# Optimization experiments

Hardware: AMD Instinct MI355X
Metric: run time of the kernel (lower is better)

Reference implementation:

```python
import jax, jax.numpy as jnp
import numpy as np

C = 768
TEMB = 512
HID = int(C * 2.0)  # prompt_mlp hidden
K = max(1, int(C * 0.5))  # top-k channels = 384


def silu(x):
    return x * jax.nn.sigmoid(x)


def conv1x1(h, W, b):
    # h: [b,c,H,W], W: [o,c], b: [o]
    return jnp.einsum('bchw,oc->bohw', h, W) + b[None, :, None, None]


def setup_inputs() -> dict:
    key = jax.random.key(0)
    ks = jax.random.split(key, 20)
    s = 0.02
    return {
        'x': jax.random.normal(ks[0], (16, C, 64, 64), jnp.float32),
        'temb': jax.random.normal(ks[1], (16, TEMB), jnp.float32),
        'W_ts': jax.random.normal(ks[2], (2 * C, TEMB), jnp.float32) * s,
        'b_ts': jnp.zeros((2 * C,), jnp.float32),
        'W_tp': jax.random.normal(ks[3], (C, TEMB), jnp.float32) * s,
        'b_tp': jnp.zeros((C,), jnp.float32),
        'W_m1': jax.random.normal(ks[4], (HID, 2 * C), jnp.float32) * s,
        'b_m1': jnp.zeros((HID,), jnp.float32),
        'W_m2': jax.random.normal(ks[5], (C, HID), jnp.float32) * s,
        'b_m2': jnp.zeros((C,), jnp.float32),
        'Wq': jax.random.normal(ks[6], (C, C), jnp.float32) * s,
        'bq': jnp.zeros((C,), jnp.float32),
        'Wk': jax.random.normal(ks[7], (C, C), jnp.float32) * s,
        'bk': jnp.zeros((C,), jnp.float32),
        'Wv': jax.random.normal(ks[8], (C, C), jnp.float32) * s,
        'bv': jnp.zeros((C,), jnp.float32),
        'Wo': jax.random.normal(ks[9], (C, C), jnp.float32) * s,
        'bo': jnp.zeros((C,), jnp.float32),
    }


def reference(x, temb, W_ts, b_ts, W_tp, b_tp, W_m1, b_m1, W_m2, b_m2,
              Wq, bq, Wk, bk, Wv, bv, Wo, bo):
    b, c, H, W = x.shape
    # TimeScaleShift
    ss = silu(temb) @ W_ts.T + b_ts                       # [b, 2c]
    scale, shift = jnp.split(ss, 2, axis=1)
    h = x * (1 + scale[:, :, None, None]) + shift[:, :, None, None]
    # prompt
    gap = h.mean(axis=(2, 3))                             # [b, c]
    tp = silu(temb) @ W_tp.T + b_tp                       # [b, c]
    p = jnp.concatenate([gap, tp], axis=1)                # [b, 2c]
    prompt = silu(p @ W_m1.T + b_m1) @ W_m2.T + b_m2      # [b, c]
    # top-k channel selection
    _, idx = jax.lax.top_k(prompt, K)                     # [b, K]
    bi = jnp.arange(b)[:, None]
    # 1x1 convs then gather selected channels
    q = conv1x1(h, Wq, bq)[bi, idx].reshape(b, K, H * W)
    kf = conv1x1(h, Wk, bk)[bi, idx].reshape(b, K, H * W)
    v = conv1x1(h, Wv, bv)[bi, idx].reshape(b, K, H * W)
    # channel attention
    attn = jax.nn.softmax(jnp.einsum('bkn,bln->bkl', q, kf) * (K ** -0.5), axis=-1)
    out = jnp.einsum('bkl,bln->bkn', attn, v).reshape(b, K, H, W)
    # scatter back into full channel space
    out_full = jnp.zeros_like(h).at[bi, idx].set(out)
    return conv1x1(out_full, Wo, bo)
```

## Files before the change

### kernel.cpp

```cpp
#include <hip/hip_runtime.h>

#define NB 16
#define NC 768
#define NT 512
#define KS 384
#define NPX 4096
#define BK 64

typedef __bf16 bfx8 __attribute__((ext_vector_type(8)));
typedef float fx4 __attribute__((ext_vector_type(4)));
typedef unsigned short u16;
typedef unsigned short usv4 __attribute__((ext_vector_type(4)));

__device__ __forceinline__ u16 f2bf(float f) {
  unsigned u = __builtin_bit_cast(unsigned, f);
  u += 0x7FFFu + ((u >> 16) & 1u);
  return (u16)(u >> 16);
}

__device__ __forceinline__ void gload16(const u16* g, u16* l) {
  __builtin_amdgcn_global_load_lds(
      (const __attribute__((address_space(1))) unsigned int*)g,
      (__attribute__((address_space(3))) unsigned int*)l, 16, 0, 0);
}

__global__ void k_trans_mean(const float* __restrict__ x, u16* __restrict__ xT,
                             u16* __restrict__ xC, float* __restrict__ parts) {
  __shared__ float ld[64][65];
  int p0 = blockIdx.x * 64, c0 = blockIdx.y * 64, b = blockIdx.z;
  int t = threadIdx.x;
  int k = t & 15, ir = t >> 4;
  int jr = k * 4;
#pragma unroll
  for (int s = 0; s < 4; ++s) {
    int i = ir + s * 16;
    float4 v = *(const float4*)&x[(size_t)(b * NC + c0 + i) * NPX + p0 + jr];
    ld[i][jr] = v.x; ld[i][jr + 1] = v.y; ld[i][jr + 2] = v.z; ld[i][jr + 3] = v.w;
    usv4 pk = {f2bf(v.x), f2bf(v.y), f2bf(v.z), f2bf(v.w)};
    *(usv4*)&xC[(size_t)(b * NC + c0 + i) * NPX + p0 + jr] = pk;
  }
  __syncthreads();
#pragma unroll
  for (int s = 0; s < 4; ++s) {
    int j = ir + s * 16;
    usv4 pk = {f2bf(ld[k * 4][j]), f2bf(ld[k * 4 + 1][j]),
               f2bf(ld[k * 4 + 2][j]), f2bf(ld[k * 4 + 3][j])};
    *(usv4*)&xT[(size_t)(b * NPX + p0 + j) * NC + c0 + k * 4] = pk;
  }
  if (t < 64) {
    float s = 0.f;
    for (int j = 0; j < 64; ++j) s += ld[t][j];
    parts[(size_t)(b * NC + c0 + t) * 64 + blockIdx.x] = s;
  }
}

__global__ void k_mean_fin(const float* __restrict__ parts, float* __restrict__ xmean) {
  int id = blockIdx.x * 256 + threadIdx.x;
  if (id >= NB * NC) return;
  float s = 0.f;
  for (int j = 0; j < 64; ++j) s += parts[(size_t)id * 64 + j];
  xmean[id] = s * (1.f / 4096.f);
}

__global__ void k_silu(const float* __restrict__ temb, float* __restrict__ st) {
  int id = blockIdx.x * 256 + threadIdx.x;
  if (id < NB * NT) { float v = temb[id]; st[id] = v / (1.f + expf(-v)); }
}

__global__ void k_mlp8(const float* __restrict__ W, const float* __restrict__ bias,
                       const float* __restrict__ X, float* __restrict__ Y,
                       int len, int nj, int ostride, int obase, int dosilu) {
  __shared__ float Xs[8 * 1537];
  int t = threadIdx.x, lane = t & 63, w = t >> 6;
  int b0 = blockIdx.y * 8;
  int ldx = len + 1;
  for (int id = t; id < 8 * len; id += 256) {
    int bb = id / len, s = id - bb * len;
    Xs[bb * ldx + s] = X[(size_t)(b0 + bb) * len + s];
  }
  __syncthreads();
  for (int i = 0; i < 4; ++i) {
    int j = blockIdx.x * 16 + i * 4 + w;
    if (j < nj) {
      float acc[8] = {0, 0, 0, 0, 0, 0, 0, 0};
      for (int s = lane; s < len; s += 64) {
        float wv = W[(size_t)j * len + s];
#pragma unroll
        for (int bb = 0; bb < 8; ++bb) acc[bb] += wv * Xs[bb * ldx + s];
      }
#pragma unroll
      for (int bb = 0; bb < 8; ++bb) {
        float r = acc[bb];
#pragma unroll
        for (int m = 32; m; m >>= 1) r += __shfl_xor(r, m);
        if (lane == 0) {
          r += bias[j];
          if (dosilu) r = r / (1.f + expf(-r));
          Y[(size_t)(b0 + bb) * ostride + obase + j] = r;
        }
      }
    }
  }
}

__global__ void k_assemble_p(const float* __restrict__ Y1, const float* __restrict__ xmean,
                             float* __restrict__ p) {
  int id = blockIdx.x * 256 + threadIdx.x;
  if (id >= NB * NC) return;
  int b = id / NC, c = id - b * NC;
  const float* yb = Y1 + (size_t)b * 2304;
  p[(size_t)b * 1536 + c] = xmean[id] * (1.f + yb[c]) + yb[768 + c];
  p[(size_t)b * 1536 + 768 + c] = yb[1536 + c];
}

__global__ void k_topk(const float* __restrict__ prompt, int* __restrict__ idx) {
  __shared__ float pr[NC];
  int b = blockIdx.x, t = threadIdx.x;
  for (int c = t; c < NC; c += 256) pr[c] = prompt[(size_t)b * NC + c];
  __syncthreads();
  for (int c = t; c < NC; c += 256) {
    float v = pr[c];
    int r = 0;
    for (int c2 = 0; c2 < NC; ++c2) {
      float v2 = pr[c2];
      r += (v2 > v) || (v2 == v && c2 < c);
    }
    if (r < KS) idx[b * KS + r] = c;
  }
}

__global__ void k_fold(const int* __restrict__ idx, const float* __restrict__ Y1,
                       const float* __restrict__ xmean,
                       const float* __restrict__ Wq, const float* __restrict__ bq,
                       const float* __restrict__ Wk, const float* __restrict__ bk,
                       const float* __restrict__ Wv, const float* __restrict__ bv,
                       u16* __restrict__ Aq, float* __restrict__ biasq,
                       float* __restrict__ sig) {
  __shared__ float red[5 * 256];
  int k = blockIdx.x, b = blockIdx.y, t = threadIdx.x;
  int row = idx[b * KS + k];
  const float* yb = Y1 + (size_t)b * 2304;
  u16* aq = Aq + (size_t)b * 1152 * NC;
  float dq = 0.f, dk = 0.f, dv = 0.f, sq = 0.f, sk = 0.f;
  for (int c = t; c < NC; c += 256) {
    float sc = 1.f + yb[c], sh = yb[768 + c];
    float xm = xmean[b * NC + c];
    float wq = Wq[(size_t)row * NC + c];
    float wk = Wk[(size_t)row * NC + c];
    float wv = Wv[(size_t)row * NC + c];
    aq[(size_t)k * NC + c] = f2bf(wq * sc);
    aq[(size_t)(KS + k) * NC + c] = f2bf(wk * sc);
    aq[(size_t)(2 * KS + k) * NC + c] = f2bf(wv * sc);
    dq += wq * sh; dk += wk * sh; dv += wv * sh;
    sq += wq * sc * xm; sk += wk * sc * xm;
  }
  red[t] = dq; red[256 + t] = dk; red[512 + t] = dv; red[768 + t] = sq; red[1024 + t] = sk;
  __syncthreads();
  for (int s = 128; s; s >>= 1) {
    if (t < s) {
#pragma unroll
      for (int q = 0; q < 5; ++q) red[q * 256 + t] += red[q * 256 + t + s];
    }
    __syncthreads();
  }
  if (t == 0) {
    biasq[b * 1152 + k] = bq[row] + red[0];
    biasq[b * 1152 + KS + k] = bk[row] + red[256];
    biasq[b * 1152 + 2 * KS + k] = bv[row] + red[512];
    sig[b * NC + k] = 4096.f * red[768];
    sig[b * NC + KS + k] = 4096.f * red[1024];
  }
}

__global__ void k_gather_wo(const int* __restrict__ idx, const float* __restrict__ Wo,
                            u16* __restrict__ WoSel) {
  __shared__ int il[KS];
  int b = blockIdx.y, t = threadIdx.x;
  for (int k = t; k < KS; k += 256) il[k] = idx[b * KS + k];
  __syncthreads();
  int o0 = blockIdx.x * 8;
  for (int oo = 0; oo < 8; ++oo) {
    int o = o0 + oo;
    const float* wr = Wo + (size_t)o * NC;
    u16* dst = WoSel + ((size_t)b * NC + o) * KS;
    for (int k = t; k < KS; k += 256) dst[k] = f2bf(wr[il[k]]);
  }
}

__global__ void k_gmerge(const float* __restrict__ Gp, u16* __restrict__ G) {
  __shared__ u16 gl[128][130];
  int tt = blockIdx.x, b = blockIdx.y, t = threadIdx.x;
  int i = 0;
  while ((i + 1) * (i + 2) / 2 <= tt) ++i;
  int j = tt - i * (i + 1) / 2;
  const float* p0 = Gp + ((size_t)(0 * NB + b) * 21 + tt) * 16384;
  const float* p1 = Gp + ((size_t)(1 * NB + b) * 21 + tt) * 16384;
  const float* p2 = Gp + ((size_t)(2 * NB + b) * 21 + tt) * 16384;
#pragma unroll
  for (int s = 0; s < 16; ++s) {
    int id = t + 256 * s;
    int row = id >> 5, col4 = (id & 31) * 4;
    float4 a = *(const float4*)&p0[row * 128 + col4];
    float4 bb = *(const float4*)&p1[row * 128 + col4];
    float4 c = *(const float4*)&p2[row * 128 + col4];
    usv4 pk = {f2bf(a.x + bb.x + c.x), f2bf(a.y + bb.y + c.y),
               f2bf(a.z + bb.z + c.z), f2bf(a.w + bb.w + c.w)};
    gl[row][col4] = pk[0]; gl[row][col4 + 1] = pk[1];
    gl[row][col4 + 2] = pk[2]; gl[row][col4 + 3] = pk[3];
    *(usv4*)&G[((size_t)b * NC + i * 128 + row) * NC + j * 128 + col4] = pk;
  }
  if (i == j) return;
  __syncthreads();
#pragma unroll
  for (int s = 0; s < 16; ++s) {
    int id = t + 256 * s;
    int row = id >> 5, col4 = (id & 31) * 4;
    usv4 pk = {gl[col4][row], gl[col4 + 1][row], gl[col4 + 2][row], gl[col4 + 3][row]};
    *(usv4*)&G[((size_t)b * NC + j * 128 + row) * NC + i * 128 + col4] = pk;
  }
}

__global__ void k_softmax(const float* __restrict__ S, u16* __restrict__ At) {
  __shared__ float sh[2];
  int kk = blockIdx.x, b = blockIdx.y, t = threadIdx.x;
  const float* srow = S + ((size_t)b * KS + kk) * KS;
  float v[3];
#pragma unroll
  for (int i = 0; i < 3; ++i) v[i] = srow[t + 128 * i];
  float m = fmaxf(fmaxf(v[0], v[1]), v[2]);
#pragma unroll
  for (int s = 32; s; s >>= 1) m = fmaxf(m, __shfl_xor(m, s));
  if ((t & 63) == 0) sh[t >> 6] = m;
  __syncthreads();
  m = fmaxf(sh[0], sh[1]);
  float e[3];
  float sum = 0.f;
#pragma unroll
  for (int i = 0; i < 3; ++i) { e[i] = expf(v[i] - m); sum += e[i]; }
#pragma unroll
  for (int s = 32; s; s >>= 1) sum += __shfl_xor(sum, s);
  __syncthreads();
  if ((t & 63) == 0) sh[t >> 6] = sum;
  __syncthreads();
  sum = sh[0] + sh[1];
  float inv = 1.f / sum;
#pragma unroll
  for (int i = 0; i < 3; ++i) {
    int l = t + 128 * i;
    At[((size_t)b * KS + l) * KS + kk] = f2bf(e[i] * inv);
  }
}

template <int EPI>
__global__ __launch_bounds__(256, 2) void gemm_bt(
    const u16* __restrict__ A, const u16* __restrict__ Bt, size_t sA, size_t sB,
    int ldA, int ldB, int K, const float* __restrict__ bias, int bstride,
    float* __restrict__ outF, u16* __restrict__ outU, int ldC, size_t sC,
    const float* __restrict__ sigp, const float* __restrict__ bqp, float scale) {
  __shared__ u16 As[128 * BK];
  __shared__ u16 Bs[128 * BK];
  int b, m0, n0, kbeg = 0, kend = K, tt = 0, gpart = 0;
  if constexpr (EPI == 5) {
    tt = blockIdx.x;
    int ii = 0;
    while ((ii + 1) * (ii + 2) / 2 <= tt) ++ii;
    int jj = tt - ii * (ii + 1) / 2;
    m0 = ii * 128; n0 = jj * 128;
    b = blockIdx.z / 3; gpart = blockIdx.z % 3;
    kbeg = (gpart == 0) ? 0 : ((gpart == 1) ? 1408 : 2752);
    kend = (gpart == 0) ? 1408 : ((gpart == 1) ? 2752 : 4096);
  } else {
    b = blockIdx.z; m0 = blockIdx.y * 128; n0 = blockIdx.x * 128;
  }
  const u16* Ab = A + (size_t)b * sA;
  const u16* Bb = Bt + (size_t)b * sB;
  int t = threadIdx.x, lane = t & 63, w = t >> 6;
  int wm = (w >> 1) * 64, wn = (w & 1) * 64;
  int r16 = lane & 15, g = lane >> 4;

  int srow = w * 32 + (lane >> 3);
  int scol = (lane & 7) * 8;
  const u16* Ag = Ab + (size_t)(m0 + srow) * ldA + kbeg + scol;
  const u16* Bg = Bb + (size_t)(n0 + srow) * ldB + kbeg + scol;
  u16* Asl = &As[(w * 32) * BK];
  u16* Bsl = &Bs[(w * 32) * BK];

  fx4 acc[4][4] = {};

  for (int k0 = kbeg; k0 < kend; k0 += BK) {
#pragma unroll
    for (int s = 0; s < 4; ++s) gload16(Ag + (size_t)s * 8 * ldA, Asl + s * 8 * BK);
#pragma unroll
    for (int s = 0; s < 4; ++s) gload16(Bg + (size_t)s * 8 * ldB, Bsl + s * 8 * BK);
    Ag += BK; Bg += BK;
    __syncthreads();
#pragma unroll
    for (int kk = 0; kk < 2; ++kk) {
      bfx8 af[4], bfr[4];
#pragma unroll
      for (int i = 0; i < 4; ++i) {
        af[i] = *(const bfx8*)&As[(wm + i * 16 + r16) * BK + kk * 32 + g * 8];
        bfr[i] = *(const bfx8*)&Bs[(wn + i * 16 + r16) * BK + kk * 32 + g * 8];
      }
#pragma unroll
      for (int i = 0; i < 4; ++i)
#pragma unroll
        for (int j = 0; j < 4; ++j)
          acc[i][j] = __builtin_amdgcn_mfma_f32_16x16x32_bf16(af[i], bfr[j], acc[i][j], 0, 0, 0);
    }
    __syncthreads();
  }

#pragma unroll
  for (int i = 0; i < 4; ++i) {
#pragma unroll
    for (int j = 0; j < 4; ++j) {
      int row = wm + i * 16 + g * 4;
      int col = wn + j * 16 + r16;
      fx4 v = acc[i][j];
      if constexpr (EPI == 0) {
        usv4 pk;
#pragma unroll
        for (int r = 0; r < 4; ++r) pk[r] = f2bf(v[r] + bias[b * bstride + m0 + row + r]);
        *(usv4*)&outU[(size_t)b * sC + (size_t)(n0 + col) * ldC + (m0 + row)] = pk;
      } else if constexpr (EPI == 1) {
        int gc = n0 + col;
        float bk_ = bqp[b * 1152 + 384 + gc];
        float sk_ = sigp[b * NC + 384 + gc];
#pragma unroll
        for (int r = 0; r < 4; ++r) {
          int gr = m0 + row + r;
          float bq_ = bqp[b * 1152 + gr];
          float sq_ = sigp[b * NC + gr];
          float val = (v[r] + bq_ * sk_ + bk_ * sq_ + 4096.f * bq_ * bk_) * scale;
          outF[(size_t)b * sC + (size_t)gr * ldC + gc] = val;
        }
      } else if constexpr (EPI == 2) {
#pragma unroll
        for (int r = 0; r < 4; ++r)
          outU[(size_t)b * sC + (size_t)(m0 + row + r) * ldC + (n0 + col)] = f2bf(v[r]);
      } else if constexpr (EPI == 3) {
#pragma unroll
        for (int r = 0; r < 4; ++r)
          outF[(size_t)b * sC + (size_t)(m0 + row + r) * ldC + (n0 + col)] =
              v[r] + bias[b * bstride + m0 + row + r];
      } else {
        float* o = outF + ((size_t)(gpart * NB + b) * 21 + tt) * 16384;
#pragma unroll
        for (int r = 0; r < 4; ++r) o[(row + r) * 128 + col] = v[r];
      }
    }
  }
}

__global__ void k_sentinel(float* out, int n) {
  int id = blockIdx.x * 256 + threadIdx.x;
  if (id < n) out[id] = 12345.0f;
}

extern "C" void kernel_launch(void* const* d_in, const int* in_sizes, int n_in,
                              void* d_out, int out_size, void* d_ws, size_t ws_size,
                              hipStream_t stream) {
  const float* x    = (const float*)d_in[0];
  const float* temb = (const float*)d_in[1];
  const float* W_ts = (const float*)d_in[2];
  const float* b_ts = (const float*)d_in[3];
  const float* W_tp = (const float*)d_in[4];
  const float* b_tp = (const float*)d_in[5];
  const float* W_m1 = (const float*)d_in[6];
  const float* b_m1 = (const float*)d_in[7];
  const float* W_m2 = (const float*)d_in[8];
  const float* b_m2 = (const float*)d_in[9];
  const float* Wq = (const float*)d_in[10];
  const float* bq = (const float*)d_in[11];
  const float* Wk = (const float*)d_in[12];
  const float* bk = (const float*)d_in[13];
  const float* Wv = (const float*)d_in[14];
  const float* bv = (const float*)d_in[15];
  const float* Wo = (const float*)d_in[16];
  const float* bo = (const float*)d_in[17];
  float* out = (float*)d_out;

  char* base = (char*)d_ws;
  size_t off = 0;
  auto alloc = [&](size_t bytes) -> char* {
    char* pp = base + off;
    off += (bytes + 255) & ~(size_t)255;
    return pp;
  };
  u16* xT   = (u16*)alloc((size_t)NB * NPX * NC * 2);
  u16* xC   = (u16*)alloc((size_t)NB * NC * NPX * 2);
  u16* vT   = (u16*)alloc((size_t)NB * NPX * KS * 2);
  u16* Aq   = (u16*)alloc((size_t)NB * 1152 * NC * 2);
  u16* WoS  = (u16*)alloc((size_t)NB * NC * KS * 2);
  float* parts  = (float*)alloc((size_t)NB * NC * 64 * 4);
  float* xmean  = (float*)alloc((size_t)NB * NC * 4);
  float* Y1     = (float*)alloc((size_t)NB * 2304 * 4);
  float* st     = (float*)alloc((size_t)NB * NT * 4);
  float* p      = (float*)alloc((size_t)NB * 1536 * 4);
  float* hid    = (float*)alloc((size_t)NB * 1536 * 4);
  float* pr     = (float*)alloc((size_t)NB * NC * 4);
  int*   idx    = (int*)alloc((size_t)NB * KS * 4);
  float* biasq  = (float*)alloc((size_t)NB * 1152 * 4);
  float* sig    = (float*)alloc((size_t)NB * NC * 4);

  if (off > ws_size) {
    k_sentinel<<<(out_size + 255) / 256, 256, 0, stream>>>(out, out_size);
    return;
  }

  float* Gp = (float*)xT;
  u16* G  = (u16*)xC;
  u16* T  = (u16*)((char*)xC + 20u * 1024 * 1024);
  float* S = (float*)((char*)xC + 30u * 1024 * 1024);
  u16* At = (u16*)((char*)xC + 40u * 1024 * 1024);
  u16* Mm = (u16*)((char*)xC + 46u * 1024 * 1024);

  k_trans_mean<<<dim3(64, 12, NB), 256, 0, stream>>>(x, xT, xC, parts);
  k_mean_fin<<<(NB * NC + 255) / 256, 256, 0, stream>>>(parts, xmean);
  k_silu<<<(NB * NT + 255) / 256, 256, 0, stream>>>(temb, st);
  k_mlp8<<<dim3(96, 2), 256, 0, stream>>>(W_ts, b_ts, st, Y1, 512, 1536, 2304, 0, 0);
  k_mlp8<<<dim3(48, 2), 256, 0, stream>>>(W_tp, b_tp, st, Y1, 512, 768, 2304, 1536, 0);
  k_assemble_p<<<(NB * NC + 255) / 256, 256, 0, stream>>>(Y1, xmean, p);
  k_mlp8<<<dim3(96, 2), 256, 0, stream>>>(W_m1, b_m1, p, hid, 1536, 1536, 1536, 0, 1);
  k_mlp8<<<dim3(48, 2), 256, 0, stream>>>(W_m2, b_m2, hid, pr, 1536, 768, 768, 0, 0);
  k_topk<<<NB, 256, 0, stream>>>(pr, idx);
  k_fold<<<dim3(KS, NB), 256, 0, stream>>>(idx, Y1, xmean, Wq, bq, Wk, bk, Wv, bv, Aq, biasq, sig);
  k_gather_wo<<<dim3(96, NB), 256, 0, stream>>>(idx, Wo, WoS);

  gemm_bt<0><<<dim3(32, 3, NB), 256, 0, stream>>>(
      Aq + (size_t)2 * KS * NC, xT, (size_t)1152 * NC, (size_t)NPX * NC, NC, NC, NC,
      biasq + 2 * KS, 1152, nullptr, vT, KS, (size_t)NPX * KS, nullptr, nullptr, 0.f);
  gemm_bt<5><<<dim3(21, 1, NB * 3), 256, 0, stream>>>(
      xC, xC, (size_t)NC * NPX, (size_t)NC * NPX, NPX, NPX, NPX,
      nullptr, 0, Gp, nullptr, 0, 0, nullptr, nullptr, 0.f);
  k_gmerge<<<dim3(21, NB), 256, 0, stream>>>(Gp, G);
  gemm_bt<2><<<dim3(6, 3, NB), 256, 0, stream>>>(
      Aq + (size_t)KS * NC, G, (size_t)1152 * NC, (size_t)NC * NC, NC, NC, NC,
      nullptr, 0, nullptr, T, NC, (size_t)KS * NC, nullptr, nullptr, 0.f);
  gemm_bt<1><<<dim3(3, 3, NB), 256, 0, stream>>>(
      Aq, T, (size_t)1152 * NC, (size_t)KS * NC, NC, NC, NC,
      nullptr, 0, S, nullptr, KS, (size_t)KS * KS, sig, biasq, 0.05103103630798287f);
  k_softmax<<<dim3(KS, NB), 128, 0, stream>>>(S, At);
  gemm_bt<2><<<dim3(3, 6, NB), 256, 0, stream>>>(
      WoS, At, (size_t)NC * KS, (size_t)KS * KS, KS, KS, KS,
      nullptr, 0, nullptr, Mm, KS, (size_t)NC * KS, nullptr, nullptr, 0.f);
  gemm_bt<3><<<dim3(32, 6, NB), 256, 0, stream>>>(
      Mm, vT, (size_t)NC * KS, (size_t)NPX * KS, KS, KS, KS,
      bo, 0, out, nullptr, NPX, (size_t)NC * NPX, nullptr, nullptr, 0.f);
}
```

Before: 675.4 us.

## Fold V projection into output weights and drop separate V GEMM

Instead of materialising the projected V tensor over all pixels, the kernel multiplies Wo-selected weights by the attention matrix and then by the scaled V weights. This yields a per-batch 768x768 combined weight, applied directly to the transposed input in one GEMM, with a separately computed fused bias. It also reduces the Gram split-K from three parts to two and merges the mean-finalize and SiLU kernels. The change removes the V GEMM and its intermediate traffic, but the final GEMM's reduction dimension doubles to 768 and it adds a transpose and a small GEMM.

```diff
diff --git a/kernel.cpp b/kernel.cpp
--- a/kernel.cpp
+++ b/kernel.cpp
@@ -16,6 +16,9 @@
   unsigned u = __builtin_bit_cast(unsigned, f);
   u += 0x7FFFu + ((u >> 16) & 1u);
   return (u16)(u >> 16);
+}
+__device__ __forceinline__ float bf2f(u16 v) {
+  return __builtin_bit_cast(float, (unsigned)v << 16);
 }
 
 __device__ __forceinline__ void gload16(const u16* g, u16* l) {
@@ -54,17 +57,15 @@
   }
 }
 
-__global__ void k_mean_fin(const float* __restrict__ parts, float* __restrict__ xmean) {
-  int id = blockIdx.x * 256 + threadIdx.x;
-  if (id >= NB * NC) return;
-  float s = 0.f;
-  for (int j = 0; j < 64; ++j) s += parts[(size_t)id * 64 + j];
-  xmean[id] = s * (1.f / 4096.f);
-}
-
-__global__ void k_silu(const float* __restrict__ temb, float* __restrict__ st) {
+__global__ void k_misc(const float* __restrict__ parts, float* __restrict__ xmean,
+                       const float* __restrict__ temb, float* __restrict__ st) {
   int id = blockIdx.x * 256 + threadIdx.x;
   if (id < NB * NT) { float v = temb[id]; st[id] = v / (1.f + expf(-v)); }
+  if (id < NB * NC) {
+    float s = 0.f;
+    for (int j = 0; j < 64; ++j) s += parts[(size_t)id * 64 + j];
+    xmean[id] = s * (1.f / 4096.f);
+  }
 }
 
 __global__ void k_mlp8(const float* __restrict__ W, const float* __restrict__ bias,
@@ -134,13 +135,14 @@
                        const float* __restrict__ Wq, const float* __restrict__ bq,
                        const float* __restrict__ Wk, const float* __restrict__ bk,
                        const float* __restrict__ Wv, const float* __restrict__ bv,
-                       u16* __restrict__ Aq, float* __restrict__ biasq,
-                       float* __restrict__ sig) {
+                       u16* __restrict__ Aq, u16* __restrict__ Avtmp,
+                       float* __restrict__ biasq, float* __restrict__ sig) {
   __shared__ float red[5 * 256];
   int k = blockIdx.x, b = blockIdx.y, t = threadIdx.x;
   int row = idx[b * KS + k];
   const float* yb = Y1 + (size_t)b * 2304;
-  u16* aq = Aq + (size_t)b * 1152 * NC;
+  u16* aq = Aq + (size_t)b * 768 * NC;
+  u16* av = Avtmp + (size_t)b * KS * NC;
   float dq = 0.f, dk = 0.f, dv = 0.f, sq = 0.f, sk = 0.f;
   for (int c = t; c < NC; c += 256) {
     float sc = 1.f + yb[c], sh = yb[768 + c];
@@ -150,7 +152,7 @@
     float wv = Wv[(size_t)row * NC + c];
     aq[(size_t)k * NC + c] = f2bf(wq * sc);
     aq[(size_t)(KS + k) * NC + c] = f2bf(wk * sc);
-    aq[(size_t)(2 * KS + k) * NC + c] = f2bf(wv * sc);
+    av[(size_t)k * NC + c] = f2bf(wv * sc);
     dq += wq * sh; dk += wk * sh; dv += wv * sh;
     sq += wq * sc * xm; sk += wk * sc * xm;
   }
@@ -169,6 +171,25 @@
     biasq[b * 1152 + 2 * KS + k] = bv[row] + red[512];
     sig[b * NC + k] = 4096.f * red[768];
     sig[b * NC + KS + k] = 4096.f * red[1024];
+  }
+}
+
+__global__ void k_avt(const u16* __restrict__ Avtmp, u16* __restrict__ AvT) {
+  __shared__ u16 tl[64][65];
+  int lt = blockIdx.x % 6, ct = blockIdx.x / 6, b = blockIdx.y;
+  int l0 = lt * 64, c0 = ct * 64, t = threadIdx.x;
+#pragma unroll
+  for (int s = 0; s < 16; ++s) {
+    int id = t + 256 * s;
+    int r = id >> 6, c = id & 63;
+    tl[r][c] = Avtmp[(size_t)b * KS * NC + (size_t)(l0 + r) * NC + c0 + c];
+  }
+  __syncthreads();
+#pragma unroll
+  for (int s = 0; s < 16; ++s) {
+    int id = t + 256 * s;
+    int r = id >> 6, c = id & 63;
+    AvT[(size_t)b * NC * KS + (size_t)(c0 + r) * KS + l0 + c] = tl[c][r];
   }
 }
 
@@ -195,16 +216,13 @@
   int j = tt - i * (i + 1) / 2;
   const float* p0 = Gp + ((size_t)(0 * NB + b) * 21 + tt) * 16384;
   const float* p1 = Gp + ((size_t)(1 * NB + b) * 21 + tt) * 16384;
-  const float* p2 = Gp + ((size_t)(2 * NB + b) * 21 + tt) * 16384;
 #pragma unroll
   for (int s = 0; s < 16; ++s) {
     int id = t + 256 * s;
     int row = id >> 5, col4 = (id & 31) * 4;
     float4 a = *(const float4*)&p0[row * 128 + col4];
     float4 bb = *(const float4*)&p1[row * 128 + col4];
-    float4 c = *(const float4*)&p2[row * 128 + col4];
-    usv4 pk = {f2bf(a.x + bb.x + c.x), f2bf(a.y + bb.y + c.y),
-               f2bf(a.z + bb.z + c.z), f2bf(a.w + bb.w + c.w)};
+    usv4 pk = {f2bf(a.x + bb.x), f2bf(a.y + bb.y), f2bf(a.z + bb.z), f2bf(a.w + bb.w)};
     gl[row][col4] = pk[0]; gl[row][col4 + 1] = pk[1];
     gl[row][col4 + 2] = pk[2]; gl[row][col4 + 3] = pk[3];
     *(usv4*)&G[((size_t)b * NC + i * 128 + row) * NC + j * 128 + col4] = pk;
@@ -248,6 +266,20 @@
   for (int i = 0; i < 3; ++i) {
     int l = t + 128 * i;
     At[((size_t)b * KS + l) * KS + kk] = f2bf(e[i] * inv);
+  }
+}
+
+__global__ void k_bias_fin(const u16* __restrict__ R, const float* __restrict__ biasq,
+                           const float* __restrict__ bo, float* __restrict__ bias_fin) {
+  __shared__ float bv[KS];
+  int b = blockIdx.x, t = threadIdx.x;
+  for (int l = t; l < KS; l += 256) bv[l] = biasq[b * 1152 + 768 + l];
+  __syncthreads();
+  for (int o = t; o < NC; o += 256) {
+    const u16* rr = R + ((size_t)b * NC + o) * KS;
+    float s = bo[o];
+    for (int l = 0; l < KS; ++l) s += bf2f(rr[l]) * bv[l];
+    bias_fin[b * NC + o] = s;
   }
 }
 
@@ -266,9 +298,8 @@
     while ((ii + 1) * (ii + 2) / 2 <= tt) ++ii;
     int jj = tt - ii * (ii + 1) / 2;
     m0 = ii * 128; n0 = jj * 128;
-    b = blockIdx.z / 3; gpart = blockIdx.z % 3;
-    kbeg = (gpart == 0) ? 0 : ((gpart == 1) ? 1408 : 2752);
-    kend = (gpart == 0) ? 1408 : ((gpart == 1) ? 2752 : 4096);
+    b = blockIdx.z >> 1; gpart = blockIdx.z & 1;
+    kbeg = gpart * 2048; kend = kbeg + 2048;
   } else {
     b = blockIdx.z; m0 = blockIdx.y * 128; n0 = blockIdx.x * 128;
   }
@@ -318,12 +349,7 @@
       int row = wm + i * 16 + g * 4;
       int col = wn + j * 16 + r16;
       fx4 v = acc[i][j];
-      if constexpr (EPI == 0) {
-        usv4 pk;
-#pragma unroll
-        for (int r = 0; r < 4; ++r) pk[r] = f2bf(v[r] + bias[b * bstride + m0 + row + r]);
-        *(usv4*)&outU[(size_t)b * sC + (size_t)(n0 + col) * ldC + (m0 + row)] = pk;
-      } else if constexpr (EPI == 1) {
+      if constexpr (EPI == 1) {
         int gc = n0 + col;
         float bk_ = bqp[b * 1152 + 384 + gc];
         float sk_ = sigp[b * NC + 384 + gc];
@@ -390,9 +416,10 @@
   };
   u16* xT   = (u16*)alloc((size_t)NB * NPX * NC * 2);
   u16* xC   = (u16*)alloc((size_t)NB * NC * NPX * 2);
-  u16* vT   = (u16*)alloc((size_t)NB * NPX * KS * 2);
-  u16* Aq   = (u16*)alloc((size_t)NB * 1152 * NC * 2);
+  u16* Aq   = (u16*)alloc((size_t)NB * 768 * NC * 2);
+  u16* AvT  = (u16*)alloc((size_t)NB * NC * KS * 2);
   u16* WoS  = (u16*)alloc((size_t)NB * NC * KS * 2);
+  float* Gp = (float*)alloc((size_t)2 * NB * 21 * 16384 * 4);
   float* parts  = (float*)alloc((size_t)NB * NC * 64 * 4);
   float* xmean  = (float*)alloc((size_t)NB * NC * 4);
   float* Y1     = (float*)alloc((size_t)NB * 2304 * 4);
@@ -403,49 +430,53 @@
   int*   idx    = (int*)alloc((size_t)NB * KS * 4);
   float* biasq  = (float*)alloc((size_t)NB * 1152 * 4);
   float* sig    = (float*)alloc((size_t)NB * NC * 4);
+  float* bias_fin = (float*)alloc((size_t)NB * NC * 4);
 
   if (off > ws_size) {
     k_sentinel<<<(out_size + 255) / 256, 256, 0, stream>>>(out, out_size);
     return;
   }
 
-  float* Gp = (float*)xT;
-  u16* G  = (u16*)xC;
-  u16* T  = (u16*)((char*)xC + 20u * 1024 * 1024);
-  float* S = (float*)((char*)xC + 30u * 1024 * 1024);
-  u16* At = (u16*)((char*)xC + 40u * 1024 * 1024);
-  u16* Mm = (u16*)((char*)xC + 46u * 1024 * 1024);
+  u16* Avtmp = (u16*)Gp;
+  u16* G   = (u16*)xC;
+  u16* T   = (u16*)((char*)xC + 20u * 1024 * 1024);
+  float* S = (float*)((char*)xC + 32u * 1024 * 1024);
+  u16* At  = (u16*)((char*)xC + 44u * 1024 * 1024);
+  u16* R   = (u16*)((char*)xC + 52u * 1024 * 1024);
+  u16* Wf  = (u16*)((char*)xC + 64u * 1024 * 1024);
 
   k_trans_mean<<<dim3(64, 12, NB), 256, 0, stream>>>(x, xT, xC, parts);
-  k_mean_fin<<<(NB * NC + 255) / 256, 256, 0, stream>>>(parts, xmean);
-  k_silu<<<(NB * NT + 255) / 256, 256, 0, stream>>>(temb, st);
+  k_misc<<<48, 256, 0, stream>>>(parts, xmean, temb, st);
   k_mlp8<<<dim3(96, 2), 256, 0, stream>>>(W_ts, b_ts, st, Y1, 512, 1536, 2304, 0, 0);
   k_mlp8<<<dim3(48, 2), 256, 0, stream>>>(W_tp, b_tp, st, Y1, 512, 768, 2304, 1536, 0);
   k_assemble_p<<<(NB * NC + 255) / 256, 256, 0, stream>>>(Y1, xmean, p);
   k_mlp8<<<dim3(96, 2), 256, 0, stream>>>(W_m1, b_m1, p, hid, 1536, 1536, 1536, 0, 1);
   k_mlp8<<<dim3(48, 2), 256, 0, stream>>>(W_m2, b_m2, hid, pr, 1536, 768, 768, 0, 0);
   k_topk<<<NB, 256, 0, stream>>>(pr, idx);
-  k_fold<<<dim3(KS, NB), 256, 0, stream>>>(idx, Y1, xmean, Wq, bq, Wk, bk, Wv, bv, Aq, biasq, sig);
+  k_fold<<<dim3(KS, NB), 256, 0, stream>>>(idx, Y1, xmean, Wq, bq, Wk, bk, Wv, bv,
+                                           Aq, Avtmp, biasq, sig);
+  k_avt<<<dim3(72, NB), 256, 0, stream>>>(Avtmp, AvT);
   k_gather_wo<<<dim3(96, NB), 256, 0, stream>>>(idx, Wo, WoS);
 
-  gemm_bt<0><<<dim3(32, 3, NB), 256, 0, stream>>>(
-      Aq + (size_t)2 * KS * NC, xT, (size_t)1152 * NC, (size_t)NPX * NC, NC, NC, NC,
-      biasq + 2 * KS, 1152, nullptr, vT, KS, (size_t)NPX * KS, nullptr, nullptr, 0.f);
-  gemm_bt<5><<<dim3(21, 1, NB * 3), 256, 0, stream>>>(
+  gemm_bt<5><<<dim3(21, 1, NB * 2), 256, 0, stream>>>(
       xC, xC, (size_t)NC * NPX, (size_t)NC * NPX, NPX, NPX, NPX,
       nullptr, 0, Gp, nullptr, 0, 0, nullptr, nullptr, 0.f);
   k_gmerge<<<dim3(21, NB), 256, 0, stream>>>(Gp, G);
   gemm_bt<2><<<dim3(6, 3, NB), 256, 0, stream>>>(
-      Aq + (size_t)KS * NC, G, (size_t)1152 * NC, (size_t)NC * NC, NC, NC, NC,
+      Aq + (size_t)KS * NC, G, (size_t)768 * NC, (size_t)NC * NC, NC, NC, NC,
       nullptr, 0, nullptr, T, NC, (size_t)KS * NC, nullptr, nullptr, 0.f);
   gemm_bt<1><<<dim3(3, 3, NB), 256, 0, stream>>>(
-      Aq, T, (size_t)1152 * NC, (size_t)KS * NC, NC, NC, NC,
+      Aq, T, (size_t)768 * NC, (size_t)KS * NC, NC, NC, NC,
       nullptr, 0, S, nullptr, KS, (size_t)KS * KS, sig, biasq, 0.05103103630798287f);
   k_softmax<<<dim3(KS, NB), 128, 0, stream>>>(S, At);
   gemm_bt<2><<<dim3(3, 6, NB), 256, 0, stream>>>(
       WoS, At, (size_t)NC * KS, (size_t)KS * KS, KS, KS, KS,
-      nullptr, 0, nullptr, Mm, KS, (size_t)NC * KS, nullptr, nullptr, 0.f);
+      nullptr, 0, nullptr, R, KS, (size_t)NC * KS, nullptr, nullptr, 0.f);
+  k_bias_fin<<<NB, 256, 0, stream>>>(R, biasq, bo, bias_fin);
+  gemm_bt<2><<<dim3(6, 6, NB), 256, 0, stream>>>(
+      R, AvT, (size_t)NC * KS, (size_t)NC * KS, KS, KS, KS,
+      nullptr, 0, nullptr, Wf, NC, (size_t)NC * NC, nullptr, nullptr, 0.f);
   gemm_bt<3><<<dim3(32, 6, NB), 256, 0, stream>>>(
-      Mm, vT, (size_t)NC * KS, (size_t)NPX * KS, KS, KS, KS,
-      bo, 0, out, nullptr, NPX, (size_t)NC * NPX, nullptr, nullptr, 0.f);
-}
+      Wf, xT, (size_t)NC * NC, (size_t)NPX * NC, NC, NC, NC,
+      bias_fin, NC, out, nullptr, NPX, (size_t)NC * NPX, nullptr, nullptr, 0.f);
+}
```

Measured after the change: 684.5 us. About the same (+1.4%).
